# Kernel optimization log

Measured on AMD Instinct MI355X. Metric: run time of the kernel, lower is better.

Reference implementation:

```python
import jax, jax.numpy as jnp
import numpy as np

D_MODEL = 1024
SEQ_LEN = 2048
NUM_EIGH = 24
BATCH = 4


def _spectral_filters(L, K):
    # Hankel matrix Z[i,j] = 2 / ((i+j)^3 - (i+j)), 1-indexed; top-K eigvecs scaled by sigma^0.25
    t = np.arange(1, L + 1, dtype=np.float64)
    s = t[:, None] + t[None, :]
    Z = 2.0 / (s ** 3 - s)
    sigma, phi = np.linalg.eigh(Z)
    phi_k = phi[:, -K:] * (sigma[-K:] ** 0.25)
    return jnp.asarray(phi_k, dtype=jnp.float32)


def setup_inputs() -> dict:
    key = jax.random.key(0)
    k1, k2, k3 = jax.random.split(key, 3)
    std = 1.0 / np.sqrt(D_MODEL)
    return {
        "x": jax.random.normal(k1, (BATCH, SEQ_LEN, D_MODEL), dtype=jnp.float32),
        "M_inputs": jax.random.normal(k2, (D_MODEL, D_MODEL), dtype=jnp.float32) * std,
        "M_filters": jax.random.normal(k3, (NUM_EIGH, D_MODEL), dtype=jnp.float32) * std,
        "phi": _spectral_filters(SEQ_LEN, NUM_EIGH),
    }


def _convolve_approx(u, v, n):
    # u: [B, L, D] inputs (already projected); v: [L, D] per-channel causal filters.
    # Dual-branch causal FFT convolution:
    #   plus[b,t,d]  = sum_{s<=t} v[s,d] * u[b,t-s,d]
    #   minus[b,t,d] = (-1)^t * sum_{s<=t} v[s,d] * (-1)^{t-s} u[b,t-s,d]
    B, L, D = u.shape
    sgn = jnp.where(jnp.arange(L) % 2 == 0, 1.0, -1.0).astype(u.dtype)[None, :, None]  # [1,L,1]
    V = jnp.fft.rfft(v, n=n, axis=0)                     # [F, D] complex
    U = jnp.stack([u, u * sgn], axis=-1)                 # [B, L, D, 2]
    Uf = jnp.fft.rfft(U, n=n, axis=1)                    # [B, F, D, 2]
    conv = jnp.fft.irfft(V[None, :, :, None] * Uf, n=n, axis=1)[:, :L]  # [B, L, D, 2]
    return conv[..., 0], conv[..., 1] * sgn


def reference(x, M_inputs, M_filters, phi):
    L = x.shape[1]
    n = 1 << int(np.ceil(np.log2(2 * L - 1)))  # next pow2 of 2L-1 (static)
    x_proj = x @ M_inputs                       # [B, L, D]
    phi_proj = phi[:L] @ M_filters              # [L, D]
    spectral_plus, spectral_minus = _convolve_approx(x_proj, phi_proj, n)
    return spectral_plus + spectral_minus
```

## Files before the change

kernel.cpp:

```cpp
#include <hip/hip_runtime.h>
#include <stdint.h>

#define D_MODEL 1024
#define SEQ 2048
#define HALF 1024
#define K_EIG 24
#define GUARD4 24
#define K4 128
#define K4P (GUARD4 + K4)
#define WE_JP4 72

typedef __attribute__((ext_vector_type(8))) short bf16x8;
typedef __attribute__((ext_vector_type(4))) float f32x4;
typedef _Float16 f16;
typedef _Float16 f16x2 __attribute__((ext_vector_type(2)));
typedef unsigned int uint;

#define GAS __attribute__((address_space(1)))
#define LAS __attribute__((address_space(3)))

static __device__ __forceinline__ unsigned short f2bf(float f) {
  union { float f; uint32_t u; } v; v.f = f;
  uint32_t u = v.u;
  u += 0x7FFFu + ((u >> 16) & 1u);
  return (unsigned short)(u >> 16);
}

static __device__ __forceinline__ float dot2(uint w2, uint u2, float c) {
  return __builtin_amdgcn_fdot2(__builtin_bit_cast(f16x2, w2),
                                __builtin_bit_cast(f16x2, u2), c, false);
}

static __device__ __forceinline__ uint pkrtz(float lo, float hi) {
  return __builtin_bit_cast(uint, __builtin_amdgcn_cvt_pkrtz(lo, hi));
}

static __device__ __forceinline__ uint pkbf(float lo, float hi) {
  return (uint)f2bf(lo) | ((uint)f2bf(hi) << 16);
}

__global__ void k_zero_guard(uint4* __restrict__ u4) {
  int idx = blockIdx.x * 256 + threadIdx.x;
  int r = blockIdx.y;
  u4[(size_t)r * (K4P * 1024) + idx] = make_uint4(0u, 0u, 0u, 0u);
}

__global__ void k_transpose_M(const float* __restrict__ M, unsigned short* __restrict__ Mt) {
  __shared__ float tile[32][33];
  int k0 = blockIdx.y * 32, n0 = blockIdx.x * 32;
  int tx = threadIdx.x & 31, ty = threadIdx.x >> 5;
  #pragma unroll
  for (int r = 0; r < 32; r += 8)
    tile[ty + r][tx] = M[(size_t)(k0 + ty + r) * D_MODEL + n0 + tx];
  __syncthreads();
  #pragma unroll
  for (int r = 0; r < 32; r += 8)
    Mt[(size_t)(n0 + ty + r) * D_MODEL + k0 + tx] = f2bf(tile[tx][ty + r]);
}

__global__ __launch_bounds__(256) void k_we4(const float* __restrict__ phi,
                                             const float* __restrict__ Mf,
                                             uint4* __restrict__ we4) {
  const int jp4 = blockIdx.x;
  const int d = blockIdx.y * 256 + threadIdx.x;
  if (jp4 >= 64) {
    we4[(size_t)jp4 * D_MODEL + d] = make_uint4(0u, 0u, 0u, 0u);
    return;
  }
  __shared__ float ph[8][K_EIG];
  if (threadIdx.x < 8 * K_EIG) {
    int s = threadIdx.x / K_EIG, k = threadIdx.x - s * K_EIG;
    ph[s][k] = phi[(size_t)(16 * jp4 + 2 * s) * K_EIG + k];
  }
  __syncthreads();
  float s[8] = {};
  #pragma unroll
  for (int k = 0; k < K_EIG; ++k) {
    float mv = Mf[(size_t)k * D_MODEL + d];
    #pragma unroll
    for (int j = 0; j < 8; ++j) s[j] = fmaf(ph[j][k], mv, s[j]);
  }
  uint4 o;
  o.x = pkrtz(2.f * s[0], 2.f * s[1]);
  o.y = pkrtz(2.f * s[2], 2.f * s[3]);
  o.z = pkrtz(2.f * s[4], 2.f * s[5]);
  o.w = pkrtz(2.f * s[6], 2.f * s[7]);
  we4[(size_t)jp4 * D_MODEL + d] = o;
}

__global__ __launch_bounds__(256) void k_gemm(const float* __restrict__ X,
                                              const unsigned short* __restrict__ Bt,
                                              uint* __restrict__ Ug) {
  __shared__ unsigned short As[128 * 32];
  __shared__ unsigned short Bs[128 * 32];
  const int bid = (int)blockIdx.x;
  const int swz = (bid & 7) * 64 + (bid >> 3);
  const int m0 = (swz >> 3) * 128;
  const int n0 = (swz & 7) * 128;
  const int tid = threadIdx.x;
  const int lane = tid & 63;
  const int wave = tid >> 6;
  const int wm = wave >> 1, wn = wave & 1;
  const int srow = lane >> 2;
  const int skoff = (lane & 3) * 8;

  const int arow = tid >> 1;
  const int akh  = (tid & 1) * 16;
  const float* xsrc = X + (size_t)(m0 + arow) * 1024 + akh;
  unsigned short* adst = As + arow * 32 + akh;

  f32x4 acc[4][4] = {};

  float4 xv0 = *(const float4*)(xsrc);
  float4 xv1 = *(const float4*)(xsrc + 4);
  float4 xv2 = *(const float4*)(xsrc + 8);
  float4 xv3 = *(const float4*)(xsrc + 12);

  for (int k0 = 0; k0 < 1024; k0 += 32) {
    __syncthreads();
    #pragma unroll
    for (int c = 0; c < 2; ++c) {
      int rbase = wave * 32 + c * 16;
      const unsigned short* src = Bt + (size_t)(n0 + rbase + srow) * 1024 + k0 + skoff;
      __builtin_amdgcn_global_load_lds((const GAS void*)src, (LAS void*)(Bs + rbase * 32), 16, 0, 0);
    }
    uint4 w0, w1;
    w0.x = pkbf(xv0.x, xv0.y); w0.y = pkbf(xv0.z, xv0.w);
    w0.z = pkbf(xv1.x, xv1.y); w0.w = pkbf(xv1.z, xv1.w);
    w1.x = pkbf(xv2.x, xv2.y); w1.y = pkbf(xv2.z, xv2.w);
    w1.z = pkbf(xv3.x, xv3.y); w1.w = pkbf(xv3.z, xv3.w);
    *(uint4*)(adst) = w0;
    *(uint4*)(adst + 8) = w1;
    __syncthreads();

    {
      const int kn = (k0 + 32) & 1023;
      xv0 = *(const float4*)(xsrc + kn);
      xv1 = *(const float4*)(xsrc + kn + 4);
      xv2 = *(const float4*)(xsrc + kn + 8);
      xv3 = *(const float4*)(xsrc + kn + 12);
    }

    bf16x8 a[4], b[4];
    #pragma unroll
    for (int mt = 0; mt < 4; ++mt)
      a[mt] = *(const bf16x8*)(As + ((wm * 64 + mt * 16 + (lane & 15)) * 32 + (lane >> 4) * 8));
    #pragma unroll
    for (int nt = 0; nt < 4; ++nt)
      b[nt] = *(const bf16x8*)(Bs + ((wn * 64 + nt * 16 + (lane & 15)) * 32 + (lane >> 4) * 8));
    #pragma unroll
    for (int mt = 0; mt < 4; ++mt)
      #pragma unroll
      for (int nt = 0; nt < 4; ++nt)
        acc[mt][nt] = __builtin_amdgcn_mfma_f32_16x16x32_bf16(a[mt], b[nt], acc[mt][nt], 0, 0, 0);
  }

  const int crow = (lane >> 4) * 4;
  const int ccol = lane & 15;
  #pragma unroll
  for (int mt = 0; mt < 4; ++mt) {
    int m = m0 + wm * 64 + mt * 16 + crow;
    int b_ = m >> 11;
    int t0 = m & 2047;
    int r_e = b_ << 1;
    int k4 = t0 >> 4;
    int dwo = (t0 >> 2) & 3;
    size_t base_e = ((size_t)(r_e * K4P + GUARD4 + k4) * 1024) * 4 + dwo;
    size_t base_o = ((size_t)((r_e + 1) * K4P + GUARD4 + k4) * 1024) * 4 + dwo;
    #pragma unroll
    for (int nt = 0; nt < 4; ++nt) {
      int n = n0 + wn * 64 + nt * 16 + ccol;
      Ug[base_e + (size_t)n * 4] = pkrtz(acc[mt][nt][0], acc[mt][nt][2]);
      Ug[base_o + (size_t)n * 4] = pkrtz(acc[mt][nt][1], acc[mt][nt][3]);
    }
  }
}

__global__ __launch_bounds__(512, 6) void k_conv(const uint4* __restrict__ u4,
                                                 const uint4* __restrict__ we4,
                                                 float* __restrict__ out) {
  __shared__ uint4 u_r[32 * 64];
  __shared__ uint4 w_s[2][8][64];
  const int flat = blockIdx.x;
  const int dt = flat & 15;
  const int r  = (flat >> 4) & 7;
  const int a  = 7 - (flat >> 7);
  const int d0 = dt * 64;
  const int tid = threadIdx.x;
  const int dl = tid & 63;
  const int ig = tid >> 6;

  const uint4* ub = u4 + ((size_t)r * K4P + GUARD4) * 1024 + d0;
  const int b_ = r >> 1, p = r & 1;

#define STAGEU(k40)                                                                     \
  {                                                                                     \
    int k4e = (k40) + ig;                                                               \
    const uint4* src = ub + (long long)k4e * 1024 + dl;                                 \
    __builtin_amdgcn_global_load_lds((const GAS void*)src,                              \
                                     (LAS void*)(u_r + (k4e & 31) * 64), 16, 0, 0);     \
  }

#define STAGEW(ch)                                                                      \
  {                                                                                     \
    const uint4* src = we4 + (size_t)((ch) * 8 + ig) * 1024 + d0 + dl;                  \
    __builtin_amdgcn_global_load_lds((const GAS void*)src,                              \
                                     (LAS void*)(&w_s[(ch) & 1][ig][0]), 16, 0, 0);     \
  }

  const int i0 = a * 128;
  const int ibase = i0 + ig * 16;
  const int niter = (2 * a + 2) < 8 ? (2 * a + 2) : 8;

  STAGEU(16 * a - 8); STAGEU(16 * a); STAGEU(16 * a + 8);
  STAGEW(0);
  __syncthreads();

  float acc[16];
#pragma unroll
  for (int o = 0; o < 16; ++o) acc[o] = 0.f;

#pragma unroll 1
  for (int c = 0; c < niter; ++c) {
    STAGEU(16 * a - 8 * c - 16);
    STAGEW(c + 1);
    const int cb = c & 1;
    const int kbase = 16 * a + 2 * ig - 8 * c - 2;
#pragma unroll
    for (int s = 0; s < 4; ++s) {
      const int kb = kbase - 2 * s;
      uint4 v0 = u_r[((kb + 0) & 31) * 64 + dl];
      uint4 v1 = u_r[((kb + 1) & 31) * 64 + dl];
      uint4 v2 = u_r[((kb + 2) & 31) * 64 + dl];
      uint4 v3 = u_r[((kb + 3) & 31) * 64 + dl];
      uint P[16];
      P[0] = v0.x; P[1] = v0.y; P[2] = v0.z; P[3] = v0.w;
      P[4] = v1.x; P[5] = v1.y; P[6] = v1.z; P[7] = v1.w;
      P[8] = v2.x; P[9] = v2.y; P[10] = v2.z; P[11] = v2.w;
      P[12] = v3.x; P[13] = v3.y; P[14] = v3.z; P[15] = v3.w;
      uint4 wv0 = w_s[cb][2 * s][dl];
      uint4 wv1 = w_s[cb][2 * s + 1][dl];
      uint W[8];
      W[0] = wv0.x; W[1] = wv0.y; W[2] = wv0.z; W[3] = wv0.w;
      W[4] = wv1.x; W[5] = wv1.y; W[6] = wv1.z; W[7] = wv1.w;
      uint WS[8];
#pragma unroll
      for (int q = 0; q < 8; ++q) WS[q] = __builtin_amdgcn_alignbit(W[q], W[q], 16);
      uint pe[15];
#pragma unroll
      for (int j = 0; j < 15; ++j) pe[j] = __builtin_amdgcn_perm(P[j + 1], P[j], 0x03020504u);
#pragma unroll
      for (int q = 0; q < 8; ++q) {
#pragma unroll
        for (int h = 0; h < 8; ++h) {
          acc[2 * h]     = dot2(W[q],  pe[7 - q + h], acc[2 * h]);
          acc[2 * h + 1] = dot2(WS[q], P[8 - q + h],  acc[2 * h + 1]);
        }
      }
    }
    __syncthreads();
  }

#pragma unroll
  for (int o = 0; o < 16; ++o)
    out[((size_t)b_ * SEQ + 2 * (ibase + o) + p) * D_MODEL + d0 + dl] = acc[o];
#undef STAGEU
#undef STAGEW
}

extern "C" void kernel_launch(void* const* d_in, const int* in_sizes, int n_in,
                              void* d_out, int out_size, void* d_ws, size_t ws_size,
                              hipStream_t stream) {
  const float* x   = (const float*)d_in[0];
  const float* Mi  = (const float*)d_in[1];
  const float* Mf  = (const float*)d_in[2];
  const float* phi = (const float*)d_in[3];
  float* out = (float*)d_out;

  unsigned short* Mt = (unsigned short*)d_out;

  char* ws = (char*)d_ws;
  uint4* we4 = (uint4*)(ws);
  uint4* u4  = (uint4*)(ws + (2u << 20));

  hipLaunchKernelGGL(k_zero_guard, dim3(96, 8), dim3(256), 0, stream, u4);
  hipLaunchKernelGGL(k_transpose_M, dim3(32, 32), dim3(256), 0, stream, Mi, Mt);
  hipLaunchKernelGGL(k_we4, dim3(72, 4), dim3(256), 0, stream, phi, Mf, we4);
  hipLaunchKernelGGL(k_gemm, dim3(512), dim3(256), 0, stream, x, Mt, (uint*)u4);
  hipLaunchKernelGGL(k_conv, dim3(1024), dim3(512), 0, stream, u4, we4, out);
}
```

Baseline: 125.9 us.

## Halve conv chunk size, shrink weight LDS buffer, reorder block scheduling

The convolution kernel now processes the filter in half-size chunks (4 k4 rows per iteration instead of 8), doubling the iteration count and halving the weight double-buffer in shared memory. Block index decoding is changed so the batch/parity index varies fastest and the time-block index follows a fixed permutation, which interleaves long- and short-running blocks. Launch bounds are raised to 8 waves per SIMD to allow more resident blocks. The goal is better load balance and occupancy. The cost is more barriers per unit of work, and only half the threads issue the staging loads.

```diff
diff --git a/kernel.cpp b/kernel.cpp
--- a/kernel.cpp
+++ b/kernel.cpp
@@ -176,15 +176,16 @@
   }
 }
 
-__global__ __launch_bounds__(512, 6) void k_conv(const uint4* __restrict__ u4,
+__global__ __launch_bounds__(512, 8) void k_conv(const uint4* __restrict__ u4,
                                                  const uint4* __restrict__ we4,
                                                  float* __restrict__ out) {
   __shared__ uint4 u_r[32 * 64];
-  __shared__ uint4 w_s[2][8][64];
+  __shared__ uint4 w_s[2][4][64];
   const int flat = blockIdx.x;
-  const int dt = flat & 15;
-  const int r  = (flat >> 4) & 7;
-  const int a  = 7 - (flat >> 7);
+  const int r  = flat & 7;
+  const int k_ = flat >> 3;
+  const int a  = (int)((0x52164307u >> ((k_ & 7) * 4)) & 7u);
+  const int dt = k_ >> 3;
   const int d0 = dt * 64;
   const int tid = threadIdx.x;
   const int dl = tid & 63;
@@ -193,7 +194,7 @@
   const uint4* ub = u4 + ((size_t)r * K4P + GUARD4) * 1024 + d0;
   const int b_ = r >> 1, p = r & 1;
 
-#define STAGEU(k40)                                                                     \
+#define STAGEU8(k40)                                                                    \
   {                                                                                     \
     int k4e = (k40) + ig;                                                               \
     const uint4* src = ub + (long long)k4e * 1024 + dl;                                 \
@@ -201,19 +202,16 @@
                                      (LAS void*)(u_r + (k4e & 31) * 64), 16, 0, 0);     \
   }
 
-#define STAGEW(ch)                                                                      \
-  {                                                                                     \
-    const uint4* src = we4 + (size_t)((ch) * 8 + ig) * 1024 + d0 + dl;                  \
-    __builtin_amdgcn_global_load_lds((const GAS void*)src,                              \
-                                     (LAS void*)(&w_s[(ch) & 1][ig][0]), 16, 0, 0);     \
-  }
-
   const int i0 = a * 128;
   const int ibase = i0 + ig * 16;
-  const int niter = (2 * a + 2) < 8 ? (2 * a + 2) : 8;
-
-  STAGEU(16 * a - 8); STAGEU(16 * a); STAGEU(16 * a + 8);
-  STAGEW(0);
+  const int niter = (4 * a + 4) < 16 ? (4 * a + 4) : 16;
+
+  STAGEU8(16 * a - 8); STAGEU8(16 * a); STAGEU8(16 * a + 8);
+  if (ig < 4) {
+    const uint4* src = we4 + (size_t)ig * 1024 + d0 + dl;
+    __builtin_amdgcn_global_load_lds((const GAS void*)src,
+                                     (LAS void*)(&w_s[0][ig][0]), 16, 0, 0);
+  }
   __syncthreads();
 
   float acc[16];
@@ -222,12 +220,19 @@
 
 #pragma unroll 1
   for (int c = 0; c < niter; ++c) {
-    STAGEU(16 * a - 8 * c - 16);
-    STAGEW(c + 1);
+    if (ig < 4) {
+      int k4e = 16 * a - 4 * c - 8 + ig;
+      const uint4* usrc = ub + (long long)k4e * 1024 + dl;
+      __builtin_amdgcn_global_load_lds((const GAS void*)usrc,
+                                       (LAS void*)(u_r + (k4e & 31) * 64), 16, 0, 0);
+      const uint4* wsrc = we4 + (size_t)(4 * (c + 1) + ig) * 1024 + d0 + dl;
+      __builtin_amdgcn_global_load_lds((const GAS void*)wsrc,
+                                       (LAS void*)(&w_s[(c + 1) & 1][ig][0]), 16, 0, 0);
+    }
     const int cb = c & 1;
-    const int kbase = 16 * a + 2 * ig - 8 * c - 2;
-#pragma unroll
-    for (int s = 0; s < 4; ++s) {
+    const int kbase = 16 * a + 2 * ig - 4 * c - 2;
+#pragma unroll
+    for (int s = 0; s < 2; ++s) {
       const int kb = kbase - 2 * s;
       uint4 v0 = u_r[((kb + 0) & 31) * 64 + dl];
       uint4 v1 = u_r[((kb + 1) & 31) * 64 + dl];
@@ -264,8 +269,7 @@
 #pragma unroll
   for (int o = 0; o < 16; ++o)
     out[((size_t)b_ * SEQ + 2 * (ibase + o) + p) * D_MODEL + d0 + dl] = acc[o];
-#undef STAGEU
-#undef STAGEW
+#undef STAGEU8
 }
 
 extern "C" void kernel_launch(void* const* d_in, const int* in_sizes, int n_in,
```

New measurement: 139.3 us. 1.11x slower.
